# Performance work log

Measured on AMD Instinct MI355X. Metric: run time of the kernel, lower is better.

## Reference

```python
import jax, jax.numpy as jnp
import numpy as np

HEAD_NUM = 4
B, S, D = 8, 1024, 512


def setup_inputs() -> dict:
    k = jax.random.key(0)
    kq, kk, kv = jax.random.split(k, 3)
    return {
        "query": jax.random.normal(kq, (B, S, D), dtype=jnp.float32),
        "key": jax.random.normal(kk, (B, S, D), dtype=jnp.float32),
        "value": jax.random.normal(kv, (B, S, D), dtype=jnp.float32),
    }


def _corr_attention(q, k, v):
    # q,k,v: [B, H, S, hd]
    score = jnp.einsum('bhqd,bhkd->bhqk', q, k)  # raw dot products
    len_q = jnp.sqrt(jnp.sum(q * q, axis=-1))    # [B,H,S]
    len_k = jnp.sqrt(jnp.sum(k * k, axis=-1))    # [B,H,S]
    score = score / (len_q[..., :, None] * len_k[..., None, :])  # cosine similarity
    signal = jnp.sign(score)
    flat = jnp.abs(score).reshape(-1)            # global flatten across B,H,S,S
    n = flat.shape[0]
    idx = jnp.argsort(-flat)                     # descending sort indices
    prob = (jnp.arange(n, dtype=flat.dtype) + 1.0) / n  # (1/n, 2/n, ..., 1)
    ranked = flat.at[idx].set(prob)              # rank-transform: largest -> smallest prob
    score = (-jnp.log(ranked)).reshape(signal.shape) * signal
    return jnp.einsum('bhqk,bhkd->bhqd', score, v)


def reference(query, key, value):
    b, s, d = query.shape
    h = HEAD_NUM
    q = query.reshape(b, s, h, -1).transpose(0, 2, 1, 3)
    k = key.reshape(b, s, h, -1).transpose(0, 2, 1, 3)
    v = value.reshape(b, s, h, -1).transpose(0, 2, 1, 3)
    out = _corr_attention(q, k, v)               # [B,H,S,hd]
    return out.transpose(0, 2, 1, 3).reshape(b, s, d)
```

## Files before the change

kernel.cpp:

```cpp
#include <hip/hip_runtime.h>
#include <math.h>

#define BB 8
#define SS 1024
#define DD 512
#define HH 4
#define HD 128
#define N_SC (BB*HH*SS*SS)

#define NB 8192
#define BINS 13107.2f
#define NBLK 2048
#define NP2 64

#define OFF_S     0
#define SZ_S      ((size_t)N_SC*2)
#define OFF_QN    (OFF_S + SZ_S)
#define SZ_QN     ((size_t)BB*SS*DD*2)
#define OFF_KN    (OFF_QN + SZ_QN)
#define OFF_VT    (OFF_KN + SZ_QN)
#define OFF_PARTS (OFF_VT + SZ_QN)
#define SZ_PARTS  ((size_t)NBLK*(NB/4)*4)
#define OFF_WMAG  (OFF_PARTS + SZ_PARTS)
#define OFF_PART2 (OFF_WMAG + (size_t)NB*2)
#define OFF_CNT   (OFF_PART2 + (size_t)NP2*NB*4)

typedef __bf16 bf16x8 __attribute__((ext_vector_type(8)));
typedef float  f32x4  __attribute__((ext_vector_type(4)));
typedef unsigned short ushort_t;

__device__ __forceinline__ unsigned bf16rne(float x) {
  unsigned b = __float_as_uint(x);
  return (b + 0x7FFFu + ((b >> 16) & 1u)) >> 16;
}
__device__ __forceinline__ unsigned sbin(float s) {
  return (unsigned)fminf(fabsf(s)*BINS, 8191.0f);
}

__global__ __launch_bounds__(256) void prep_vt_kernel(
    const float* __restrict__ q, const float* __restrict__ k,
    const float* __restrict__ v,
    unsigned* __restrict__ qn, unsigned* __restrict__ kn,
    unsigned* __restrict__ vt) {
  __shared__ float T[64][65];
  int t = threadIdx.x;
  if (blockIdx.x < 8192) {
    int lane = t & 31;
    int row = blockIdx.x*8 + (t >> 5);
    const float* src; unsigned* dst; int r;
    if (row < 32768) { src = q; dst = qn; r = row; }
    else             { src = k; dst = kn; r = row - 32768; }
    int b = r >> 12, s = (r >> 2) & 1023, h = r & 3;
    float4 vv = *(const float4*)(src + ((size_t)(b*1024 + s))*512 + h*128 + lane*4);
    float sum = vv.x*vv.x + vv.y*vv.y + vv.z*vv.z + vv.w*vv.w;
    #pragma unroll
    for (int off = 16; off; off >>= 1) sum += __shfl_xor(sum, off, 64);
    float inv = rsqrtf(sum);
    unsigned u0 = bf16rne(vv.x*inv) | (bf16rne(vv.y*inv) << 16);
    unsigned u1 = bf16rne(vv.z*inv) | (bf16rne(vv.w*inv) << 16);
    uint2 o = {u0, u1};
    *(uint2*)&dst[(size_t)((b*4 + h)*1024 + s)*64 + lane*2] = o;
  } else {
    int vb = blockIdx.x - 8192;
    int s0 = (vb & 15)*64, d0 = ((vb >> 4) & 1)*64, bh = vb >> 5;
    int b = bh >> 2, h = bh & 3;
    #pragma unroll
    for (int i = 0; i < 16; i++) {
      int idx = t + i*256, rs = idx >> 6, cd = idx & 63;
      T[rs][cd] = v[((size_t)(b*1024 + s0 + rs))*512 + h*128 + d0 + cd];
    }
    __syncthreads();
    #pragma unroll
    for (int i = 0; i < 8; i++) {
      int idx = t + i*256, rd = idx >> 5, c2 = (idx & 31)*2;
      unsigned u = bf16rne(T[c2][rd]) | (bf16rne(T[c2+1][rd]) << 16);
      vt[(size_t)(bh*128 + d0 + rd)*512 + (s0 + c2)/2] = u;
    }
  }
}

__global__ __launch_bounds__(256) void scores_hist_kernel(
    const ushort_t* __restrict__ qn, const ushort_t* __restrict__ kn,
    ushort_t* __restrict__ S, unsigned* __restrict__ parts) {
  __shared__ ushort_t Qs[128*64];
  __shared__ ushort_t Ks[128*64];
  __shared__ unsigned h8[NB/4];
  int t = threadIdx.x;
  int L = blockIdx.x;
  int bh = L & 31, tile = L >> 5;
  int sq0 = (tile >> 3)*128, sk0 = (tile & 7)*128;

  #pragma unroll
  for (int i = 0; i < 8; i++) h8[t + i*256] = 0;

  const uint4* qg = (const uint4*)qn + (size_t)(bh*1024 + sq0)*16;
  const uint4* kg = (const uint4*)kn + (size_t)(bh*1024 + sk0)*16;

  int w = t >> 6, lane = t & 63, m16 = lane & 15, q2 = lane >> 4;
  int wm = (w >> 1)*64, wn = (w & 1)*64;
  f32x4 acc[4][4];
  #pragma unroll
  for (int i = 0; i < 4; i++)
    #pragma unroll
    for (int j = 0; j < 4; j++) acc[i][j] = (f32x4){0.f,0.f,0.f,0.f};

  #pragma unroll
  for (int kh2 = 0; kh2 < 2; kh2++) {
    #pragma unroll
    for (int i = 0; i < 4; i++) {
      int idx = t + i*256;
      int r = idx >> 3, g = idx & 7;
      *(uint4*)&Qs[r*64 + (g ^ (r & 7))*8] = qg[r*16 + kh2*8 + g];
    }
    #pragma unroll
    for (int i = 0; i < 4; i++) {
      int idx = t + i*256;
      int r = idx >> 3, g = idx & 7;
      *(uint4*)&Ks[r*64 + (g ^ (r & 7))*8] = kg[r*16 + kh2*8 + g];
    }
    __syncthreads();

    #pragma unroll
    for (int ks2 = 0; ks2 < 2; ks2++) {
      bf16x8 a[4], bb[4];
      #pragma unroll
      for (int i = 0; i < 4; i++) {
        int r = wm + i*16 + m16;
        a[i] = *(const bf16x8*)&Qs[r*64 + ((ks2*4 + q2) ^ (r & 7))*8];
      }
      #pragma unroll
      for (int j = 0; j < 4; j++) {
        int r = wn + j*16 + m16;
        bb[j] = *(const bf16x8*)&Ks[r*64 + ((ks2*4 + q2) ^ (r & 7))*8];
      }
      #pragma unroll
      for (int i = 0; i < 4; i++)
        #pragma unroll
        for (int j = 0; j < 4; j++)
          acc[i][j] = __builtin_amdgcn_mfma_f32_16x16x32_bf16(a[i], bb[j], acc[i][j], 0, 0, 0);
    }
    __syncthreads();
  }

  size_t Sbase = (size_t)bh << 20;
  #pragma unroll
  for (int i = 0; i < 4; i++)
    #pragma unroll
    for (int p = 0; p < 4; p++) {
      int row = sq0 + wm + i*16 + q2*4 + p;
      #pragma unroll
      for (int j = 0; j < 4; j++) {
        int col = sk0 + wn + j*16 + m16;
        float s = acc[i][j][p];
        unsigned bin = sbin(s);
        unsigned enc = (bin << 1) | (s < 0.f ? 1u : 0u);
        S[Sbase + ((size_t)row << 10) + col] = (ushort_t)enc;
        atomicAdd(&h8[bin >> 2], 1u << ((bin & 3)*8));
      }
    }
  __syncthreads();

  unsigned* dst = parts + (size_t)L*(NB/4);
  #pragma unroll
  for (int i = 0; i < 8; i++) dst[t + i*256] = h8[t + i*256];
}

__global__ __launch_bounds__(256) void reduce1_kernel(
    const unsigned* __restrict__ parts, unsigned* __restrict__ parts2) {
  int g = blockIdx.x*256 + threadIdx.x;
  int p0 = blockIdx.y*32;
  unsigned s0 = 0, s1 = 0, s2 = 0, s3 = 0;
  #pragma unroll 8
  for (int p = p0; p < p0 + 32; p++) {
    unsigned w = parts[(size_t)p*(NB/4) + g];
    s0 += w & 0xFFu; s1 += (w >> 8) & 0xFFu;
    s2 += (w >> 16) & 0xFFu; s3 += w >> 24;
  }
  uint4 o = {s0, s1, s2, s3};
  ((uint4*)parts2)[(size_t)blockIdx.y*(NB/4) + g] = o;
}

__global__ __launch_bounds__(256) void reduce2_kernel(
    const unsigned* __restrict__ parts2, unsigned* __restrict__ counts) {
  int g = blockIdx.x*256 + threadIdx.x;
  unsigned s = 0;
  #pragma unroll 8
  for (int p = 0; p < NP2; p++) s += parts2[(size_t)p*NB + g];
  counts[g] = s;
}

__global__ __launch_bounds__(1024) void scan_kernel(
    const unsigned* __restrict__ counts, ushort_t* __restrict__ wmag) {
  __shared__ unsigned d[1024];
  int t = threadIdx.x;
  uint4 a  = ((const uint4*)counts)[t*2];
  uint4 b2 = ((const uint4*)counts)[t*2 + 1];
  unsigned loc[8] = {a.x, a.y, a.z, a.w, b2.x, b2.y, b2.z, b2.w};
  unsigned tot = 0;
  #pragma unroll
  for (int j = 0; j < 8; j++) tot += loc[j];
  d[t] = tot; __syncthreads();
  for (int off = 1; off < 1024; off <<= 1) {
    unsigned x = (t >= off) ? d[t - off] : 0u;
    __syncthreads();
    d[t] += x;
    __syncthreads();
  }
  unsigned run = d[t] - tot;
  const float inv_n = 1.0f / (float)N_SC;
  #pragma unroll
  for (int j = 0; j < 8; j++) {
    run += loc[j];
    float rm = (float)(N_SC - run) + 0.5f*(float)(loc[j] + 1u);
    wmag[t*8 + j] = (ushort_t)bf16rne(-logf(rm * inv_n));
  }
}

__global__ __launch_bounds__(512) void out_kernel(
    const ushort_t* __restrict__ S, const ushort_t* __restrict__ wmag,
    const ushort_t* __restrict__ vt, float* __restrict__ out) {
  __shared__ ushort_t Buf[128*128 + 64*128];
  __shared__ ushort_t Wl[NB];
  ushort_t* Vs = Buf;
  ushort_t* Ss = Buf + 128*128;
  int t = threadIdx.x;
  int L = blockIdx.x;
  int bh = L & 31, q0 = (L >> 5)*64;
  int b = bh >> 2, h = bh & 3;

  #pragma unroll
  for (int i = 0; i < 2; i++)
    ((uint4*)Wl)[t + i*512] = ((const uint4*)wmag)[t + i*512];

  int w = t >> 6, lane = t & 63, m16 = lane & 15, q2 = lane >> 4;
  int qt = w & 3, kh = w >> 2;
  int qw = q0 + qt*16;
  const uint4* vg = (const uint4*)vt + (size_t)bh*128*128;
  const uint4* sg = (const uint4*)S + (size_t)bh*1024*128;

  f32x4 oacc[8];
  #pragma unroll
  for (int j = 0; j < 8; j++) oacc[j] = (f32x4){0.f,0.f,0.f,0.f};

  for (int kc = 0; kc < 8; kc++) {
    #pragma unroll
    for (int i = 0; i < 4; i++) {
      int idx = t + i*512, row = idx >> 4, g = idx & 15;
      *(uint4*)&Vs[row*128 + (g ^ (row & 15))*8] = vg[row*128 + kc*16 + g];
    }
    #pragma unroll
    for (int i = 0; i < 2; i++) {
      int idx = t + i*512, row = idx >> 4, g = idx & 15;
      *(uint4*)&Ss[row*128 + (g ^ (row & 15))*8] = sg[(size_t)(q0 + row)*128 + kc*16 + g];
    }
    __syncthreads();

    #pragma unroll
    for (int u = 0; u < 2; u++) {
      int gk = kh*8 + u*4 + q2;
      uint4 sv = *(const uint4*)&Ss[(qt*16 + m16)*128 + (gk ^ m16)*8];
      unsigned sc[4] = {sv.x, sv.y, sv.z, sv.w};
      union { bf16x8 v; unsigned u2[4]; } af;
      #pragma unroll
      for (int m = 0; m < 4; m++) {
        unsigned elo = sc[m] & 0xFFFFu;
        unsigned ehi = sc[m] >> 16;
        unsigned wlo = (unsigned)Wl[elo >> 1] | ((elo & 1u) << 15);
        unsigned whi = (unsigned)Wl[ehi >> 1] | ((ehi & 1u) << 15);
        af.u2[m] = wlo | (whi << 16);
      }
      #pragma unroll
      for (int j = 0; j < 8; j++) {
        bf16x8 bb = *(const bf16x8*)&Vs[(j*16 + m16)*128 + (gk ^ m16)*8];
        oacc[j] = __builtin_amdgcn_mfma_f32_16x16x32_bf16(af.v, bb, oacc[j], 0, 0, 0);
      }
    }
    __syncthreads();
  }

  float* R = (float*)Buf;
  if (kh == 1) {
    #pragma unroll
    for (int j = 0; j < 8; j++)
      #pragma unroll
      for (int p = 0; p < 4; p++)
        R[(qt*16 + q2*4 + p)*129 + j*16 + m16] = oacc[j][p];
  }
  __syncthreads();
  if (kh == 0) {
    #pragma unroll
    for (int j = 0; j < 8; j++)
      #pragma unroll
      for (int p = 0; p < 4; p++)
        oacc[j][p] += R[(qt*16 + q2*4 + p)*129 + j*16 + m16];
    #pragma unroll
    for (int p = 0; p < 4; p++) {
      int qrow = qw + q2*4 + p;
      #pragma unroll
      for (int j = 0; j < 8; j++)
        out[(size_t)(b*1024 + qrow)*512 + h*128 + j*16 + m16] = oacc[j][p];
    }
  }
}

extern "C" void kernel_launch(void* const* d_in, const int* in_sizes, int n_in,
                              void* d_out, int out_size, void* d_ws, size_t ws_size,
                              hipStream_t stream) {
  const float* q = (const float*)d_in[0];
  const float* k = (const float*)d_in[1];
  const float* v = (const float*)d_in[2];
  float* out = (float*)d_out;
  char* ws = (char*)d_ws;

  ushort_t* Sbuf  = (ushort_t*)(ws + OFF_S);
  unsigned* qn    = (unsigned*)(ws + OFF_QN);
  unsigned* kn    = (unsigned*)(ws + OFF_KN);
  unsigned* vtb   = (unsigned*)(ws + OFF_VT);
  unsigned* parts = (unsigned*)(ws + OFF_PARTS);
  ushort_t* wmag  = (ushort_t*)(ws + OFF_WMAG);
  unsigned* part2 = (unsigned*)(ws + OFF_PART2);
  unsigned* cnt   = (unsigned*)(ws + OFF_CNT);

  hipLaunchKernelGGL(prep_vt_kernel, dim3(9216), dim3(256), 0, stream, q, k, v, qn, kn, vtb);
  hipLaunchKernelGGL(scores_hist_kernel, dim3(NBLK), dim3(256), 0, stream,
                     (const ushort_t*)qn, (const ushort_t*)kn, Sbuf, parts);
  hipLaunchKernelGGL(reduce1_kernel, dim3(8, NP2), dim3(256), 0, stream, parts, part2);
  hipLaunchKernelGGL(reduce2_kernel, dim3(32), dim3(256), 0, stream, part2, cnt);
  hipLaunchKernelGGL(scan_kernel, dim3(1), dim3(1024), 0, stream, cnt, wmag);
  hipLaunchKernelGGL(out_kernel, dim3(512), dim3(512), 0, stream,
                     (const ushort_t*)Sbuf, wmag, (const ushort_t*)vtb, out);
}
```

Before: 154.4 us.

## Fuse first histogram reduction into scores kernel via global atomics

Each scores block now atomically adds its nonzero per-bin shared-memory counts into one of 64 global partial histograms, selected by block index mod 64. This replaces writing a full per-block partial histogram and removes the separate reduce1 kernel. The 64 partial buffers are zeroed by extra blocks appended to the prep kernel. This cuts a 16 MB partial write and reread plus one launch, in exchange for up to 32-way global atomic contention per bin.

```diff
diff --git a/kernel.cpp b/kernel.cpp
--- a/kernel.cpp
+++ b/kernel.cpp
@@ -41,7 +41,7 @@
     const float* __restrict__ q, const float* __restrict__ k,
     const float* __restrict__ v,
     unsigned* __restrict__ qn, unsigned* __restrict__ kn,
-    unsigned* __restrict__ vt) {
+    unsigned* __restrict__ vt, unsigned* __restrict__ part2) {
   __shared__ float T[64][65];
   int t = threadIdx.x;
   if (blockIdx.x < 8192) {
@@ -60,7 +60,7 @@
     unsigned u1 = bf16rne(vv.z*inv) | (bf16rne(vv.w*inv) << 16);
     uint2 o = {u0, u1};
     *(uint2*)&dst[(size_t)((b*4 + h)*1024 + s)*64 + lane*2] = o;
-  } else {
+  } else if (blockIdx.x < 9216) {
     int vb = blockIdx.x - 8192;
     int s0 = (vb & 15)*64, d0 = ((vb >> 4) & 1)*64, bh = vb >> 5;
     int b = bh >> 2, h = bh & 3;
@@ -76,12 +76,18 @@
       unsigned u = bf16rne(T[c2][rd]) | (bf16rne(T[c2+1][rd]) << 16);
       vt[(size_t)(bh*128 + d0 + rd)*512 + (s0 + c2)/2] = u;
     }
+  } else {
+    int zb = blockIdx.x - 9216;
+    uint4 z = {0u, 0u, 0u, 0u};
+    #pragma unroll
+    for (int i = 0; i < 8; i++)
+      ((uint4*)part2)[(size_t)zb*(NB/4) + t + i*256] = z;
   }
 }
 
 __global__ __launch_bounds__(256) void scores_hist_kernel(
     const ushort_t* __restrict__ qn, const ushort_t* __restrict__ kn,
-    ushort_t* __restrict__ S, unsigned* __restrict__ parts) {
+    ushort_t* __restrict__ S, unsigned* __restrict__ part2) {
   __shared__ ushort_t Qs[128*64];
   __shared__ ushort_t Ks[128*64];
   __shared__ unsigned h8[NB/4];
@@ -160,24 +166,20 @@
     }
   __syncthreads();
 
-  unsigned* dst = parts + (size_t)L*(NB/4);
-  #pragma unroll
-  for (int i = 0; i < 8; i++) dst[t + i*256] = h8[t + i*256];
-}
-
-__global__ __launch_bounds__(256) void reduce1_kernel(
-    const unsigned* __restrict__ parts, unsigned* __restrict__ parts2) {
-  int g = blockIdx.x*256 + threadIdx.x;
-  int p0 = blockIdx.y*32;
-  unsigned s0 = 0, s1 = 0, s2 = 0, s3 = 0;
-  #pragma unroll 8
-  for (int p = p0; p < p0 + 32; p++) {
-    unsigned w = parts[(size_t)p*(NB/4) + g];
-    s0 += w & 0xFFu; s1 += (w >> 8) & 0xFFu;
-    s2 += (w >> 16) & 0xFFu; s3 += w >> 24;
-  }
-  uint4 o = {s0, s1, s2, s3};
-  ((uint4*)parts2)[(size_t)blockIdx.y*(NB/4) + g] = o;
+  unsigned* dst = part2 + (size_t)(L & 63)*NB;
+  #pragma unroll
+  for (int i = 0; i < 8; i++) {
+    unsigned wd = h8[t + i*256];
+    if (wd) {
+      int base = (t + i*256)*4;
+      unsigned c0 = wd & 0xFFu, c1 = (wd >> 8) & 0xFFu;
+      unsigned c2 = (wd >> 16) & 0xFFu, c3 = wd >> 24;
+      if (c0) atomicAdd(&dst[base + 0], c0);
+      if (c1) atomicAdd(&dst[base + 1], c1);
+      if (c2) atomicAdd(&dst[base + 2], c2);
+      if (c3) atomicAdd(&dst[base + 3], c3);
+    }
+  }
 }
 
 __global__ __launch_bounds__(256) void reduce2_kernel(
@@ -316,15 +318,14 @@
   unsigned* qn    = (unsigned*)(ws + OFF_QN);
   unsigned* kn    = (unsigned*)(ws + OFF_KN);
   unsigned* vtb   = (unsigned*)(ws + OFF_VT);
-  unsigned* parts = (unsigned*)(ws + OFF_PARTS);
   ushort_t* wmag  = (ushort_t*)(ws + OFF_WMAG);
   unsigned* part2 = (unsigned*)(ws + OFF_PART2);
   unsigned* cnt   = (unsigned*)(ws + OFF_CNT);
 
-  hipLaunchKernelGGL(prep_vt_kernel, dim3(9216), dim3(256), 0, stream, q, k, v, qn, kn, vtb);
+  hipLaunchKernelGGL(prep_vt_kernel, dim3(9280), dim3(256), 0, stream,
+                     q, k, v, qn, kn, vtb, part2);
   hipLaunchKernelGGL(scores_hist_kernel, dim3(NBLK), dim3(256), 0, stream,
-                     (const ushort_t*)qn, (const ushort_t*)kn, Sbuf, parts);
-  hipLaunchKernelGGL(reduce1_kernel, dim3(8, NP2), dim3(256), 0, stream, parts, part2);
+                     (const ushort_t*)qn, (const ushort_t*)kn, Sbuf, part2);
   hipLaunchKernelGGL(reduce2_kernel, dim3(32), dim3(256), 0, stream, part2, cnt);
   hipLaunchKernelGGL(scan_kernel, dim3(1), dim3(1024), 0, stream, cnt, wmag);
   hipLaunchKernelGGL(out_kernel, dim3(512), dim3(512), 0, stream,
```

Measured after the change: 216.6 us. 1.4x slower.
